# Performance work log

Hardware: AMD Instinct MI355X
Metric: run time of the kernel (lower is better)

Reference implementation:

```python
import jax, jax.numpy as jnp
import numpy as np

NUM_PRODUCT = 100000
NUM_USERS = 10000
EMBED_DIM = 512
H = EMBED_DIM // 2          # gru_hidden_size = embedding_dim // 2
MBS = 20                    # max_basket_size
NB = 64                     # baskets per user
K = 256                     # batch of users
B = NB * MBS                # flattened item positions per user
L = 2                       # GRU layers


def setup_inputs() -> dict:
    key = jax.random.key(0)
    ks = jax.random.split(key, 8)
    filter_basket_prob = jax.random.uniform(ks[0], (K, B), dtype=jnp.float32)
    # item ids in [-1, NUM_PRODUCT-1]; -1 is padding (shifted to padding_idx 0)
    input_seq_tensor = jax.random.randint(ks[1], (K, B), 0, NUM_PRODUCT + 1) - 1
    uid = jax.random.randint(ks[2], (K,), 0, NUM_USERS)
    embed_table = 0.02 * jax.random.normal(ks[3], (NUM_PRODUCT + 1, H), dtype=jnp.float32)
    embed_table = embed_table.at[0].set(0.0)  # padding_idx=0
    s = 1.0 / np.sqrt(H)
    w_ih = jax.random.uniform(ks[4], (L, 3 * H, H), jnp.float32, -s, s)
    w_hh = jax.random.uniform(ks[5], (L, 3 * H, H), jnp.float32, -s, s)
    b_ih = jax.random.uniform(ks[6], (L, 3 * H), jnp.float32, -s, s)
    b_hh = jax.random.uniform(ks[7], (L, 3 * H), jnp.float32, -s, s)
    return {"filter_basket_prob": filter_basket_prob, "input_seq_tensor": input_seq_tensor,
            "uid": uid, "embed_table": embed_table,
            "w_ih": w_ih, "w_hh": w_hh, "b_ih": b_ih, "b_hh": b_hh}


def _gru_layer(x, wih, whh, bih, bhh):
    # x: [K, T, H]; torch GRU gate math (r, z, n gate order)
    gi = jnp.einsum('kth,gh->ktg', x, wih) + bih  # [K, T, 3H]

    def step(h, gi_t):
        gh = h @ whh.T + bhh
        ir, iz, inn = jnp.split(gi_t, 3, axis=-1)
        hr, hz, hn = jnp.split(gh, 3, axis=-1)
        r = jax.nn.sigmoid(ir + hr)
        z = jax.nn.sigmoid(iz + hz)
        n = jnp.tanh(inn + r * hn)
        h_new = (1.0 - z) * n + z * h
        return h_new, h_new

    h0 = jnp.zeros((x.shape[0], whh.shape[1]), x.dtype)
    _, hs = jax.lax.scan(step, h0, jnp.swapaxes(gi, 0, 1))  # [T, K, H]
    return jnp.swapaxes(hs, 0, 1)


def reference(filter_basket_prob, input_seq_tensor, uid, embed_table, w_ih, w_hh, b_ih, b_hh):
    Kb, Bb = filter_basket_prob.shape
    Hh = embed_table.shape[1]
    nb = Bb // MBS
    # mask out padding positions (constant w.r.t. grads, as in torch .detach())
    mask = (input_seq_tensor != -1).astype(jnp.float32)
    prob = filter_basket_prob * mask                      # [K, B]
    emb = embed_table[input_seq_tensor + 1]               # [K, B, H]
    emb_f = (emb * prob[..., None]).reshape(Kb, nb, MBS, Hh)
    prob_b = prob.reshape(Kb, nb, MBS)
    filter_b = prob_b.max(axis=-1)                        # [K, NB]
    # avg basket pooling: sum(prob*emb) / (sum(prob) + eps)
    basket_emb = emb_f.sum(axis=2) / (prob_b.sum(axis=-1, keepdims=True) + 1e-10)
    valid = (filter_b > 0).astype(jnp.int32)
    # stable descending sort moves valid baskets to the front, preserving order
    order = jnp.argsort(-valid, axis=-1)                  # [K, NB]
    lengths = valid.sum(axis=-1)
    lengths = lengths + (lengths == 0).astype(lengths.dtype)  # clamp to >= 1
    x = jnp.take_along_axis(basket_emb, order[:, :, None], axis=1)  # [K, NB, H]
    # pack/pad/unsort in the original cancel out: GRU output at t depends only
    # on inputs <= t, so run the full padded scan and read step lengths-1.
    for l in range(w_ih.shape[0]):
        x = _gru_layer(x, w_ih[l], w_hh[l], b_ih[l], b_hh[l])
    return x[jnp.arange(Kb), lengths - 1]                 # [K, H]
```

## Files before the change

### kernel.cpp

```cpp
#include <hip/hip_runtime.h>
#include <cstdint>

#define KU 256
#define NBASK 64
#define MBS 20
#define BITEMS 1280
#define HD 256
#define G3 768
#define TT 64

typedef short v8s __attribute__((ext_vector_type(8)));
typedef float v4f __attribute__((ext_vector_type(4)));
typedef unsigned short v4us __attribute__((ext_vector_type(4)));
typedef unsigned int v4u __attribute__((ext_vector_type(4)));

__device__ __forceinline__ unsigned short f2b(float f){
  uint32_t u = __float_as_uint(f);
  u += 0x7FFFu + ((u >> 16) & 1u);
  return (unsigned short)(u >> 16);
}
__device__ __forceinline__ float b2f(unsigned short s){
  return __uint_as_float(((uint32_t)s) << 16);
}
__device__ __forceinline__ unsigned int packf(float x){
  unsigned short hi = f2b(x);
  unsigned short lo = f2b(x - b2f(hi));
  return ((unsigned int)hi << 16) | lo;
}
__device__ __forceinline__ float unpackf(unsigned int v){
  return b2f((unsigned short)(v >> 16)) + b2f((unsigned short)(v & 0xffffu));
}
__device__ __forceinline__ void waitflag(int* f, int v){
  while (__hip_atomic_load(f, __ATOMIC_ACQUIRE, __HIP_MEMORY_SCOPE_AGENT) < v)
    __builtin_amdgcn_s_sleep(2);
}

__global__ __launch_bounds__(1024) void k_convert(
    const float* __restrict__ wih, const float* __restrict__ whh,
    unsigned short* __restrict__ wih1hi, unsigned short* __restrict__ wih1lo,
    unsigned short* __restrict__ wih2hi, unsigned short* __restrict__ wih2lo,
    unsigned short* __restrict__ whh1hi, unsigned short* __restrict__ whh1lo,
    unsigned short* __restrict__ whh2hi, unsigned short* __restrict__ whh2lo)
{
  int idx = blockIdx.x * 1024 + threadIdx.x;
  int which = blockIdx.y;
  float v;
  if (which == 0)      v = wih[idx];
  else if (which == 1) v = wih[196608 + idx];
  else if (which == 2) v = whh[idx];
  else                 v = whh[196608 + idx];
  unsigned short hi = f2b(v);
  unsigned short lo = f2b(v - b2f(hi));
  if (which == 0)      { wih1hi[idx] = hi; wih1lo[idx] = lo; }
  else if (which == 1) { wih2hi[idx] = hi; wih2lo[idx] = lo; }
  else if (which == 2) { whh1hi[idx] = hi; whh1lo[idx] = lo; }
  else                 { whh2hi[idx] = hi; whh2lo[idx] = lo; }
}

__global__ void k_zero(int* flags){
  if (threadIdx.x < 96) flags[threadIdx.x] = 0;
}

__global__ __launch_bounds__(64) void k_order(
    const float* __restrict__ prob, const int* __restrict__ seq,
    int* __restrict__ order, int* __restrict__ lengths)
{
  int k = blockIdx.x, j = threadIdx.x;
  int base = k * BITEMS + j * MBS;
  float mx = 0.f;
  #pragma unroll
  for (int m = 0; m < MBS; m++) {
    int it = seq[base + m];
    float p = (it >= 0) ? prob[base + m] : 0.f;
    mx = fmaxf(mx, p);
  }
  bool valid = mx > 0.f;
  unsigned long long bal = __ballot(valid);
  int len = __popcll(bal);
  unsigned long long below = bal & ((1ull << j) - 1ull);
  int pos = valid ? __popcll(below) : (len + (j - __popcll(below)));
  order[k * NBASK + j] = pos;
  if (j == 0) lengths[k] = (len > 0) ? len : 1;
}

__global__ __launch_bounds__(256) void k_basket(
    const float* __restrict__ prob, const int* __restrict__ seq,
    const float* __restrict__ table, const int* __restrict__ order,
    unsigned short* __restrict__ xbhi, unsigned short* __restrict__ xblo)
{
  int j = blockIdx.x, k = blockIdx.y;
  int h = threadIdx.x;
  int base = k * BITEMS + j * MBS;
  float acc = 0.f, sp = 0.f;
  #pragma unroll
  for (int m = 0; m < MBS; m++) {
    int it = seq[base + m];
    if (it >= 0) {
      float p = prob[base + m];
      sp += p;
      acc += p * table[(size_t)(it + 1) * HD + h];
    }
  }
  float val = acc / (sp + 1e-10f);
  int dest = order[k * NBASK + j];
  unsigned short hi = f2b(val);
  size_t o = ((size_t)k * NBASK + dest) * HD + h;
  xbhi[o] = hi;
  xblo[o] = f2b(val - b2f(hi));
}

__global__ __launch_bounds__(256) void k_gemm3(
    const unsigned short* __restrict__ Xhi, const unsigned short* __restrict__ Xlo,
    const unsigned short* __restrict__ Whi, const unsigned short* __restrict__ Wlo,
    const float* __restrict__ bias, float* __restrict__ Y)
{
  int nblk = blockIdx.x;
  int mblk = blockIdx.y;
  int wv = threadIdx.x >> 6;
  int l = threadIdx.x & 63;
  int r = l & 15, g = l >> 4;
  int mbase = mblk * 64 + wv * 16;
  int nbase = nblk * 64;
  v4f acc[4];
  #pragma unroll
  for (int c = 0; c < 4; c++) {
    float bn = bias[nbase + c * 16 + r];
    acc[c] = (v4f){bn, bn, bn, bn};
  }
  const unsigned short* xh = Xhi + (size_t)(mbase + r) * HD;
  const unsigned short* xl = Xlo + (size_t)(mbase + r) * HD;
  #pragma unroll
  for (int k0 = 0; k0 < HD; k0 += 32) {
    v8s ahi = *(const v8s*)(xh + k0 + g * 8);
    v8s alo = *(const v8s*)(xl + k0 + g * 8);
    #pragma unroll
    for (int c = 0; c < 4; c++) {
      size_t wo = (size_t)(nbase + c * 16 + r) * HD + k0 + g * 8;
      v8s bhi = *(const v8s*)(Whi + wo);
      v8s blo = *(const v8s*)(Wlo + wo);
      acc[c] = __builtin_amdgcn_mfma_f32_16x16x32_bf16(ahi, bhi, acc[c], 0, 0, 0);
      acc[c] = __builtin_amdgcn_mfma_f32_16x16x32_bf16(alo, bhi, acc[c], 0, 0, 0);
      acc[c] = __builtin_amdgcn_mfma_f32_16x16x32_bf16(ahi, blo, acc[c], 0, 0, 0);
    }
  }
  #pragma unroll
  for (int c = 0; c < 4; c++) {
    int n = nbase + c * 16 + r;
    int mrow = mbase + g * 4;
    #pragma unroll
    for (int i = 0; i < 4; i++)
      Y[(size_t)(mrow + i) * G3 + n] = acc[c][i];
  }
}

__device__ __forceinline__ void wprologue(
    const unsigned short* w0, const unsigned short* w1, const unsigned short* w2,
    int half4, v8s (&cw0)[3], v8s (&cw1)[3], v8s (&cw2)[3])
{
  #pragma unroll
  for (int q = 0; q < 3; q++) {
    int p = (half4 + q) & 7;
    cw0[q] = *(const v8s*)(w0 + p * 32);
    cw1[q] = *(const v8s*)(w1 + p * 32);
    cw2[q] = *(const v8s*)(w2 + p * 32);
  }
}
template<int K0>
__device__ __forceinline__ void mfma_quad(
    const unsigned short* __restrict__ w0, const unsigned short* __restrict__ w1,
    const unsigned short* __restrict__ w2,
    const unsigned short (*h_hi)[256], const unsigned short (*h_lo)[256],
    const unsigned short* __restrict__ nlo_s, int r, int g, int jloc, int half4,
    v8s (&cw0)[3], v8s (&cw1)[3], v8s (&cw2)[3],
    v4f& a0, v4f& a1, v4f& a2)
{
  #pragma unroll
  for (int q = 0; q < 4; q++) {
    int kidx = K0 + q;
    int buf = kidx % 3;
    int p = (half4 + kidx) & 7;
    int slotA = ((p * 4 + g) ^ (r & 7)) * 8;
    v8s ahi = *(const v8s*)&h_hi[r][slotA];
    v8s alo = *(const v8s*)&h_lo[r][slotA];
    v8s nl  = *(const v8s*)&nlo_s[jloc * 256 + slotA];
    v8s u0 = cw0[buf], u1 = cw1[buf], u2 = cw2[buf];
    if (kidx + 3 < 8) {
      int p3 = (half4 + kidx + 3) & 7;
      cw0[buf] = *(const v8s*)(w0 + p3 * 32);
      cw1[buf] = *(const v8s*)(w1 + p3 * 32);
      cw2[buf] = *(const v8s*)(w2 + p3 * 32);
    }
    a0 = __builtin_amdgcn_mfma_f32_16x16x32_bf16(ahi, u0, a0, 0, 0, 0);
    a0 = __builtin_amdgcn_mfma_f32_16x16x32_bf16(alo, u0, a0, 0, 0, 0);
    a1 = __builtin_amdgcn_mfma_f32_16x16x32_bf16(ahi, u1, a1, 0, 0, 0);
    a1 = __builtin_amdgcn_mfma_f32_16x16x32_bf16(alo, u1, a1, 0, 0, 0);
    a2 = __builtin_amdgcn_mfma_f32_16x16x32_bf16(ahi, u2, a2, 0, 0, 0);
    a2 = __builtin_amdgcn_mfma_f32_16x16x32_bf16(alo, u2, a2, 0, 0, 0);
    a2 = __builtin_amdgcn_mfma_f32_16x16x32_bf16(ahi, nl, a2, 0, 0, 0);
  }
}

__global__ __launch_bounds__(512) void k_pipe(
    const unsigned short* __restrict__ whh1hi, const unsigned short* __restrict__ whh1lo,
    const unsigned short* __restrict__ wih2hi, const unsigned short* __restrict__ wih2lo,
    const unsigned short* __restrict__ whh2hi, const unsigned short* __restrict__ whh2lo,
    float* __restrict__ gi, unsigned int* __restrict__ h1pk, unsigned int* __restrict__ h2x,
    const float* __restrict__ bhh1, const float* __restrict__ bih2,
    const float* __restrict__ bhh2,
    const int* __restrict__ lengths, float* __restrict__ out, int* flags)
{
  __shared__ unsigned short h_hi[16][256], h_lo[16][256];
  __shared__ unsigned short nlo_s[40960];
  int tid = threadIdx.x;
  int l = tid & 63, r = l & 15, g = l >> 4;
  int swv = __builtin_amdgcn_readfirstlane(tid >> 6);
  int bx = blockIdx.x;
  int role = bx >> 5, sub = bx & 31, half = sub >> 4, b = sub & 15;
  int half4 = half * 4;
  int ub = b * 16;
  int jloc = swv * 16 + r, j = half * 128 + jloc;
  int* aflag = flags, *gflag = flags + 32, *bflag = flags + 64;
  int myf = sub, sibf = sub ^ 16;

  const unsigned short* whi_g = (role == 0) ? whh1hi : (role == 1) ? wih2hi : whh2hi;
  const unsigned short* wlo_g = (role == 0) ? whh1lo : (role == 1) ? wih2lo : whh2lo;
  const float* bb_ = (role == 0) ? bhh1 : (role == 1) ? bih2 : bhh2;

  for (int idx = tid; idx < 4096; idx += 512) {
    ((unsigned short*)h_hi)[idx] = 0;
    ((unsigned short*)h_lo)[idx] = 0;
  }
  const unsigned short* wlo_n = wlo_g + 2 * 65536 + half * 128 * 256;
  for (int idx = tid; idx < 32768; idx += 512) {
    int row = idx >> 8, col = idx & 255;
    int slot = (col >> 3) ^ (row & 7);
    nlo_s[row * 256 + slot * 8 + (col & 7)] = wlo_n[idx];
  }
  const unsigned short* w0 = whi_g + (size_t)j * 256 + g * 8;
  const unsigned short* w1 = w0 + 65536;
  const unsigned short* w2 = w0 + 131072;
  float b_r = bb_[j], b_z = bb_[256 + j], b_n = bb_[512 + j];
  int sibbase = (1 - half) * 128;
  int xu = tid >> 5;
  __syncthreads();

  if (role == 0) {
    float hold[4] = {0.f, 0.f, 0.f, 0.f};
    const float* gp[4];
    unsigned int* hq[4];
    #pragma unroll
    for (int i = 0; i < 4; i++) {
      gp[i] = gi + (size_t)(ub + g * 4 + i) * TT * G3 + j;
      hq[i] = h1pk + (size_t)(ub + g * 4 + i) * TT * HD + j;
    }
    for (int t = 0; t < TT; t++) {
      float gir[4], giz[4], gin[4];
      #pragma unroll
      for (int i = 0; i < 4; i++) {
        gir[i] = gp[i][0]; giz[i] = gp[i][256]; gin[i] = gp[i][512];
        gp[i] += G3;
      }
      v8s cw0[3], cw1[3], cw2[3];
      wprologue(w0, w1, w2, half4, cw0, cw1, cw2);
      v4f a0 = {0.f,0.f,0.f,0.f}, a1 = {0.f,0.f,0.f,0.f}, a2 = {0.f,0.f,0.f,0.f};
      mfma_quad<0>(w0, w1, w2, h_hi, h_lo, nlo_s, r, g, jloc, half4, cw0, cw1, cw2, a0, a1, a2);
      if (t > 0 && tid == 0) waitflag(&aflag[sibf], t);
      __syncthreads();
      if (t > 0) {
        int sj = sibbase + (tid & 31) * 4;
        v4u pk = *(const v4u*)&h1pk[((size_t)(ub + xu) * TT + (t - 1)) * HD + sj];
        int pos = (((sj >> 3) ^ (xu & 7)) << 3) + (sj & 7);
        v4us hv, lv;
        #pragma unroll
        for (int i = 0; i < 4; i++) { hv[i] = (unsigned short)(pk[i] >> 16); lv[i] = (unsigned short)(pk[i] & 0xffffu); }
        *(v4us*)&h_hi[xu][pos] = hv;
        *(v4us*)&h_lo[xu][pos] = lv;
      }
      __syncthreads();
      mfma_quad<4>(w0, w1, w2, h_hi, h_lo, nlo_s, r, g, jloc, half4, cw0, cw1, cw2, a0, a1, a2);
      #pragma unroll
      for (int i = 0; i < 4; i++) {
        float hr = a0[i] + b_r, hz = a1[i] + b_z, hn = a2[i] + b_n;
        float rr = 1.f / (1.f + __expf(-(gir[i] + hr)));
        float zz = 1.f / (1.f + __expf(-(giz[i] + hz)));
        float e  = __expf(2.f * (gin[i] + rr * hn));
        float nn = 1.f - 2.f / (e + 1.f);
        float hnew = (1.f - zz) * nn + zz * hold[i];
        hold[i] = hnew;
        unsigned short h_  = f2b(hnew);
        unsigned short lo_ = f2b(hnew - b2f(h_));
        int u = g * 4 + i;
        int pos = (((j >> 3) ^ (u & 7)) << 3) + (j & 7);
        h_hi[u][pos] = h_;
        h_lo[u][pos] = lo_;
        hq[i][0] = ((unsigned int)h_ << 16) | lo_;
        hq[i] += HD;
      }
      __syncthreads();
      if (tid == 0) {
        __threadfence();
        __hip_atomic_store(&aflag[myf], t + 1, __ATOMIC_RELEASE, __HIP_MEMORY_SCOPE_AGENT);
      }
    }
  } else if (role == 1) {
    unsigned int* gi_u = (unsigned int*)gi;
    for (int t = 0; t < TT; t++) {
      if (tid == 0) { waitflag(&aflag[b], t + 1); waitflag(&aflag[16 + b], t + 1); }
      __syncthreads();
      {
        int c0 = (tid & 31) * 8;
        const unsigned int* src = &h1pk[((size_t)(ub + xu) * TT + t) * HD + c0];
        #pragma unroll
        for (int hf = 0; hf < 2; hf++) {
          v4u pk = *(const v4u*)(src + hf * 4);
          int sj = c0 + hf * 4;
          int pos = (((sj >> 3) ^ (xu & 7)) << 3) + (sj & 7);
          v4us hv, lv;
          #pragma unroll
          for (int i = 0; i < 4; i++) { hv[i] = (unsigned short)(pk[i] >> 16); lv[i] = (unsigned short)(pk[i] & 0xffffu); }
          *(v4us*)&h_hi[xu][pos] = hv;
          *(v4us*)&h_lo[xu][pos] = lv;
        }
      }
      __syncthreads();
      v8s cw0[3], cw1[3], cw2[3];
      wprologue(w0, w1, w2, half4, cw0, cw1, cw2);
      v4f a0 = {b_r, b_r, b_r, b_r}, a1 = {b_z, b_z, b_z, b_z}, a2 = {b_n, b_n, b_n, b_n};
      mfma_quad<0>(w0, w1, w2, h_hi, h_lo, nlo_s, r, g, jloc, half4, cw0, cw1, cw2, a0, a1, a2);
      mfma_quad<4>(w0, w1, w2, h_hi, h_lo, nlo_s, r, g, jloc, half4, cw0, cw1, cw2, a0, a1, a2);
      #pragma unroll
      for (int i = 0; i < 4; i++) {
        size_t base = ((size_t)(ub + g * 4 + i) * TT + t) * G3;
        gi_u[base + j]       = packf(a0[i]);
        gi_u[base + 256 + j] = packf(a1[i]);
        gi_u[base + 512 + j] = packf(a2[i]);
      }
      __syncthreads();
      if (tid == 0) {
        __threadfence();
        __hip_atomic_store(&gflag[myf], t + 1, __ATOMIC_RELEASE, __HIP_MEMORY_SCOPE_AGENT);
      }
    }
  } else {
    float hold[4] = {0.f, 0.f, 0.f, 0.f};
    const unsigned int* gq[4];
    int lenr[4];
    #pragma unroll
    for (int i = 0; i < 4; i++) {
      gq[i] = (const unsigned int*)gi + (size_t)(ub + g * 4 + i) * TT * G3 + j;
      lenr[i] = lengths[ub + g * 4 + i];
    }
    for (int t = 0; t < TT; t++) {
      v8s cw0[3], cw1[3], cw2[3];
      wprologue(w0, w1, w2, half4, cw0, cw1, cw2);
      v4f a0 = {0.f,0.f,0.f,0.f}, a1 = {0.f,0.f,0.f,0.f}, a2 = {0.f,0.f,0.f,0.f};
      mfma_quad<0>(w0, w1, w2, h_hi, h_lo, nlo_s, r, g, jloc, half4, cw0, cw1, cw2, a0, a1, a2);
      if (tid == 0) {
        waitflag(&gflag[myf], t + 1);
        if (t > 0) waitflag(&bflag[sibf], t);
      }
      __syncthreads();
      if (t > 0) {
        int sj = sibbase + (tid & 31) * 4;
        v4u pk = *(const v4u*)&h2x[(size_t)(ub + xu) * HD + sj];
        int pos = (((sj >> 3) ^ (xu & 7)) << 3) + (sj & 7);
        v4us hv, lv;
        #pragma unroll
        for (int i = 0; i < 4; i++) { hv[i] = (unsigned short)(pk[i] >> 16); lv[i] = (unsigned short)(pk[i] & 0xffffu); }
        *(v4us*)&h_hi[xu][pos] = hv;
        *(v4us*)&h_lo[xu][pos] = lv;
      }
      unsigned int vr[4], vz[4], vn[4];
      #pragma unroll
      for (int i = 0; i < 4; i++) {
        vr[i] = gq[i][0]; vz[i] = gq[i][256]; vn[i] = gq[i][512];
        gq[i] += G3;
      }
      __syncthreads();
      mfma_quad<4>(w0, w1, w2, h_hi, h_lo, nlo_s, r, g, jloc, half4, cw0, cw1, cw2, a0, a1, a2);
      #pragma unroll
      for (int i = 0; i < 4; i++) {
        float hr = a0[i] + b_r, hz = a1[i] + b_z, hn = a2[i] + b_n;
        float rr = 1.f / (1.f + __expf(-(unpackf(vr[i]) + hr)));
        float zz = 1.f / (1.f + __expf(-(unpackf(vz[i]) + hz)));
        float e  = __expf(2.f * (unpackf(vn[i]) + rr * hn));
        float nn = 1.f - 2.f / (e + 1.f);
        float hnew = (1.f - zz) * nn + zz * hold[i];
        hold[i] = hnew;
        unsigned short h_  = f2b(hnew);
        unsigned short lo_ = f2b(hnew - b2f(h_));
        int u = g * 4 + i;
        int pos = (((j >> 3) ^ (u & 7)) << 3) + (j & 7);
        h_hi[u][pos] = h_;
        h_lo[u][pos] = lo_;
        h2x[(size_t)(ub + u) * HD + j] = ((unsigned int)h_ << 16) | lo_;
        if (t == lenr[i] - 1)
          out[(size_t)(ub + u) * HD + j] = hnew;
      }
      __syncthreads();
      if (tid == 0) {
        __threadfence();
        __hip_atomic_store(&bflag[myf], t + 1, __ATOMIC_RELEASE, __HIP_MEMORY_SCOPE_AGENT);
      }
    }
  }
}

extern "C" void kernel_launch(void* const* d_in, const int* in_sizes, int n_in,
                              void* d_out, int out_size, void* d_ws, size_t ws_size,
                              hipStream_t stream) {
  const float* prob  = (const float*)d_in[0];
  const int*   seq   = (const int*)d_in[1];
  const float* table = (const float*)d_in[3];
  const float* wih   = (const float*)d_in[4];
  const float* whh   = (const float*)d_in[5];
  const float* bih   = (const float*)d_in[6];
  const float* bhh   = (const float*)d_in[7];
  float* out = (float*)d_out;

  char* ws = (char*)d_ws;
  float* gi            = (float*)ws;
  unsigned short* xbhi = (unsigned short*)(ws + 50331648);
  unsigned short* xblo = (unsigned short*)(ws + 58720256);
  unsigned int* h1pk   = (unsigned int*)xbhi;
  char* wsw = ws + 67108864;
  const size_t WSZ = 393216;
  unsigned short* wih1hi = (unsigned short*)(wsw + 0 * WSZ);
  unsigned short* wih1lo = (unsigned short*)(wsw + 1 * WSZ);
  unsigned short* wih2hi = (unsigned short*)(wsw + 2 * WSZ);
  unsigned short* wih2lo = (unsigned short*)(wsw + 3 * WSZ);
  unsigned short* whh1hi = (unsigned short*)(wsw + 4 * WSZ);
  unsigned short* whh1lo = (unsigned short*)(wsw + 5 * WSZ);
  unsigned short* whh2hi = (unsigned short*)(wsw + 6 * WSZ);
  unsigned short* whh2lo = (unsigned short*)(wsw + 7 * WSZ);
  int* order   = (int*)(wsw + 8 * WSZ);
  int* lengths = order + KU * NBASK;
  int* flags   = lengths + KU;
  unsigned int* h2x = (unsigned int*)wih1hi;

  k_zero<<<1, 128, 0, stream>>>(flags);
  k_convert<<<dim3(192, 4), 1024, 0, stream>>>(wih, whh,
      wih1hi, wih1lo, wih2hi, wih2lo, whh1hi, whh1lo, whh2hi, whh2lo);
  k_order<<<dim3(KU), 64, 0, stream>>>(prob, seq, order, lengths);
  k_basket<<<dim3(NBASK, KU), 256, 0, stream>>>(prob, seq, table, order, xbhi, xblo);
  k_gemm3<<<dim3(12, 256), 256, 0, stream>>>(xbhi, xblo, wih1hi, wih1lo, bih, gi);
  k_pipe<<<dim3(96), 512, 0, stream>>>(
      whh1hi, whh1lo, wih2hi, wih2lo, whh2hi, whh2lo,
      gi, h1pk, h2x, bhh, bih + G3, bhh + G3, lengths, out, flags);
}
```

Before: 712.3 us.

## Relax inter-block flag sync and prefetch layer-1 input gates into LDS

Replaces acquire loads and explicit threadfences around the cross-block flags with relaxed polling plus release stores, and reads producer data through relaxed agent-scope atomic loads instead. Layer-1 blocks now prefetch the next timestep's input-gate rows into a double-buffered shared-memory tile with coalesced vector loads, replacing per-lane strided global reads. The aim is to shorten the serial per-step latency of the pipelined GRU recurrence. Relying on relaxed ordering carries a risk of memory-ordering races, and the larger LDS footprint may affect occupancy.

```diff
diff --git a/kernel.cpp b/kernel.cpp
--- a/kernel.cpp
+++ b/kernel.cpp
@@ -31,8 +31,12 @@
   return b2f((unsigned short)(v >> 16)) + b2f((unsigned short)(v & 0xffffu));
 }
 __device__ __forceinline__ void waitflag(int* f, int v){
-  while (__hip_atomic_load(f, __ATOMIC_ACQUIRE, __HIP_MEMORY_SCOPE_AGENT) < v)
+  while (__hip_atomic_load(f, __ATOMIC_RELAXED, __HIP_MEMORY_SCOPE_AGENT) < v)
     __builtin_amdgcn_s_sleep(2);
+  asm volatile("" ::: "memory");
+}
+__device__ __forceinline__ unsigned int aload(const unsigned int* p){
+  return __hip_atomic_load(p, __ATOMIC_RELAXED, __HIP_MEMORY_SCOPE_AGENT);
 }
 
 __global__ __launch_bounds__(1024) void k_convert(
@@ -200,6 +204,28 @@
   }
 }
 
+__device__ __forceinline__ void load_gi(
+    const float* __restrict__ gi, int ub, int t, int half, int tid,
+    float (*gs)[388])
+{
+  v4f tmp[3];
+  #pragma unroll
+  for (int k = 0; k < 3; k++) {
+    int idx = k * 512 + tid;
+    int row = idx >> 5, c4 = idx & 31;
+    int u = row / 3, gate = row - u * 3;
+    tmp[k] = *(const v4f*)(gi + ((size_t)(ub + u) * TT + t) * G3
+                              + gate * 256 + half * 128 + c4 * 4);
+  }
+  #pragma unroll
+  for (int k = 0; k < 3; k++) {
+    int idx = k * 512 + tid;
+    int row = idx >> 5, c4 = idx & 31;
+    int u = row / 3, gate = row - u * 3;
+    *(v4f*)&gs[u][gate * 128 + c4 * 4] = tmp[k];
+  }
+}
+
 __global__ __launch_bounds__(512) void k_pipe(
     const unsigned short* __restrict__ whh1hi, const unsigned short* __restrict__ whh1lo,
     const unsigned short* __restrict__ wih2hi, const unsigned short* __restrict__ wih2lo,
@@ -210,7 +236,8 @@
     const int* __restrict__ lengths, float* __restrict__ out, int* flags)
 {
   __shared__ unsigned short h_hi[16][256], h_lo[16][256];
-  __shared__ unsigned short nlo_s[40960];
+  __shared__ unsigned short nlo_s[32768];
+  __shared__ float gi_s[2][16][388];
   int tid = threadIdx.x;
   int l = tid & 63, r = l & 15, g = l >> 4;
   int swv = __builtin_amdgcn_readfirstlane(tid >> 6);
@@ -246,20 +273,13 @@
 
   if (role == 0) {
     float hold[4] = {0.f, 0.f, 0.f, 0.f};
-    const float* gp[4];
     unsigned int* hq[4];
     #pragma unroll
-    for (int i = 0; i < 4; i++) {
-      gp[i] = gi + (size_t)(ub + g * 4 + i) * TT * G3 + j;
+    for (int i = 0; i < 4; i++)
       hq[i] = h1pk + (size_t)(ub + g * 4 + i) * TT * HD + j;
-    }
+    load_gi(gi, ub, 0, half, tid, gi_s[0]);
+    __syncthreads();
     for (int t = 0; t < TT; t++) {
-      float gir[4], giz[4], gin[4];
-      #pragma unroll
-      for (int i = 0; i < 4; i++) {
-        gir[i] = gp[i][0]; giz[i] = gp[i][256]; gin[i] = gp[i][512];
-        gp[i] += G3;
-      }
       v8s cw0[3], cw1[3], cw2[3];
       wprologue(w0, w1, w2, half4, cw0, cw1, cw2);
       v4f a0 = {0.f,0.f,0.f,0.f}, a1 = {0.f,0.f,0.f,0.f}, a2 = {0.f,0.f,0.f,0.f};
@@ -278,18 +298,22 @@
       }
       __syncthreads();
       mfma_quad<4>(w0, w1, w2, h_hi, h_lo, nlo_s, r, g, jloc, half4, cw0, cw1, cw2, a0, a1, a2);
+      if (t + 1 < TT) load_gi(gi, ub, t + 1, half, tid, gi_s[(t + 1) & 1]);
       #pragma unroll
       for (int i = 0; i < 4; i++) {
+        int u = g * 4 + i;
+        float ir  = gi_s[t & 1][u][jloc];
+        float iz  = gi_s[t & 1][u][128 + jloc];
+        float inn = gi_s[t & 1][u][256 + jloc];
         float hr = a0[i] + b_r, hz = a1[i] + b_z, hn = a2[i] + b_n;
-        float rr = 1.f / (1.f + __expf(-(gir[i] + hr)));
-        float zz = 1.f / (1.f + __expf(-(giz[i] + hz)));
-        float e  = __expf(2.f * (gin[i] + rr * hn));
+        float rr = 1.f / (1.f + __expf(-(ir + hr)));
+        float zz = 1.f / (1.f + __expf(-(iz + hz)));
+        float e  = __expf(2.f * (inn + rr * hn));
         float nn = 1.f - 2.f / (e + 1.f);
         float hnew = (1.f - zz) * nn + zz * hold[i];
         hold[i] = hnew;
         unsigned short h_  = f2b(hnew);
         unsigned short lo_ = f2b(hnew - b2f(h_));
-        int u = g * 4 + i;
         int pos = (((j >> 3) ^ (u & 7)) << 3) + (j & 7);
         h_hi[u][pos] = h_;
         h_lo[u][pos] = lo_;
@@ -297,10 +321,8 @@
         hq[i] += HD;
       }
       __syncthreads();
-      if (tid == 0) {
-        __threadfence();
+      if (tid == 0)
         __hip_atomic_store(&aflag[myf], t + 1, __ATOMIC_RELEASE, __HIP_MEMORY_SCOPE_AGENT);
-      }
     }
   } else if (role == 1) {
     unsigned int* gi_u = (unsigned int*)gi;
@@ -336,10 +358,8 @@
         gi_u[base + 512 + j] = packf(a2[i]);
       }
       __syncthreads();
-      if (tid == 0) {
-        __threadfence();
+      if (tid == 0)
         __hip_atomic_store(&gflag[myf], t + 1, __ATOMIC_RELEASE, __HIP_MEMORY_SCOPE_AGENT);
-      }
     }
   } else {
     float hold[4] = {0.f, 0.f, 0.f, 0.f};
@@ -362,18 +382,21 @@
       __syncthreads();
       if (t > 0) {
         int sj = sibbase + (tid & 31) * 4;
-        v4u pk = *(const v4u*)&h2x[(size_t)(ub + xu) * HD + sj];
+        const unsigned int* hx = &h2x[(size_t)(ub + xu) * HD + sj];
+        unsigned int p0 = aload(hx), p1 = aload(hx + 1), p2 = aload(hx + 2), p3 = aload(hx + 3);
         int pos = (((sj >> 3) ^ (xu & 7)) << 3) + (sj & 7);
         v4us hv, lv;
-        #pragma unroll
-        for (int i = 0; i < 4; i++) { hv[i] = (unsigned short)(pk[i] >> 16); lv[i] = (unsigned short)(pk[i] & 0xffffu); }
+        hv[0]=(unsigned short)(p0>>16); lv[0]=(unsigned short)(p0&0xffffu);
+        hv[1]=(unsigned short)(p1>>16); lv[1]=(unsigned short)(p1&0xffffu);
+        hv[2]=(unsigned short)(p2>>16); lv[2]=(unsigned short)(p2&0xffffu);
+        hv[3]=(unsigned short)(p3>>16); lv[3]=(unsigned short)(p3&0xffffu);
         *(v4us*)&h_hi[xu][pos] = hv;
         *(v4us*)&h_lo[xu][pos] = lv;
       }
       unsigned int vr[4], vz[4], vn[4];
       #pragma unroll
       for (int i = 0; i < 4; i++) {
-        vr[i] = gq[i][0]; vz[i] = gq[i][256]; vn[i] = gq[i][512];
+        vr[i] = aload(gq[i]); vz[i] = aload(gq[i] + 256); vn[i] = aload(gq[i] + 512);
         gq[i] += G3;
       }
       __syncthreads();
@@ -398,10 +421,8 @@
           out[(size_t)(ub + u) * HD + j] = hnew;
       }
       __syncthreads();
-      if (tid == 0) {
-        __threadfence();
+      if (tid == 0)
         __hip_atomic_store(&bflag[myf], t + 1, __ATOMIC_RELEASE, __HIP_MEMORY_SCOPE_AGENT);
-      }
     }
   }
 }
```

New measurement: 744.8 us. 1.05x slower.

## Split GRU pipeline K-reduction across two wave groups with LDS partial-sum merge

Applied to the files above, without the earlier changes.

The persistent pipelined GRU kernel goes from 512 to 1024 threads per block. Each recurrent matvec's K dimension is split between a front and a back group of 8 waves, and the back group's partial accumulators are reduced through a new LDS buffer before the front group does the gate math. Loading the sibling hidden state is handed to the back waves, which overlaps it with the front waves' work. The layer-2 hidden exchange buffer is double-buffered by timestep parity. This aims to shorten the serial per-step latency, at the cost of an extra __syncthreads, LDS traffic per step, and higher register pressure under launch_bounds(1024).

```diff
diff --git a/kernel.cpp b/kernel.cpp
--- a/kernel.cpp
+++ b/kernel.cpp
@@ -153,54 +153,26 @@
   }
 }
 
-__device__ __forceinline__ void wprologue(
-    const unsigned short* w0, const unsigned short* w1, const unsigned short* w2,
-    int half4, v8s (&cw0)[3], v8s (&cw1)[3], v8s (&cw2)[3])
-{
-  #pragma unroll
-  for (int q = 0; q < 3; q++) {
-    int p = (half4 + q) & 7;
-    cw0[q] = *(const v8s*)(w0 + p * 32);
-    cw1[q] = *(const v8s*)(w1 + p * 32);
-    cw2[q] = *(const v8s*)(w2 + p * 32);
-  }
-}
-template<int K0>
-__device__ __forceinline__ void mfma_quad(
-    const unsigned short* __restrict__ w0, const unsigned short* __restrict__ w1,
-    const unsigned short* __restrict__ w2,
+__device__ __forceinline__ void mfma_one(
+    int p, v8s u0, v8s u1, v8s u2,
     const unsigned short (*h_hi)[256], const unsigned short (*h_lo)[256],
-    const unsigned short* __restrict__ nlo_s, int r, int g, int jloc, int half4,
-    v8s (&cw0)[3], v8s (&cw1)[3], v8s (&cw2)[3],
+    const unsigned short* __restrict__ nlo_s, int r, int g, int jloc,
     v4f& a0, v4f& a1, v4f& a2)
 {
-  #pragma unroll
-  for (int q = 0; q < 4; q++) {
-    int kidx = K0 + q;
-    int buf = kidx % 3;
-    int p = (half4 + kidx) & 7;
-    int slotA = ((p * 4 + g) ^ (r & 7)) * 8;
-    v8s ahi = *(const v8s*)&h_hi[r][slotA];
-    v8s alo = *(const v8s*)&h_lo[r][slotA];
-    v8s nl  = *(const v8s*)&nlo_s[jloc * 256 + slotA];
-    v8s u0 = cw0[buf], u1 = cw1[buf], u2 = cw2[buf];
-    if (kidx + 3 < 8) {
-      int p3 = (half4 + kidx + 3) & 7;
-      cw0[buf] = *(const v8s*)(w0 + p3 * 32);
-      cw1[buf] = *(const v8s*)(w1 + p3 * 32);
-      cw2[buf] = *(const v8s*)(w2 + p3 * 32);
-    }
-    a0 = __builtin_amdgcn_mfma_f32_16x16x32_bf16(ahi, u0, a0, 0, 0, 0);
-    a0 = __builtin_amdgcn_mfma_f32_16x16x32_bf16(alo, u0, a0, 0, 0, 0);
-    a1 = __builtin_amdgcn_mfma_f32_16x16x32_bf16(ahi, u1, a1, 0, 0, 0);
-    a1 = __builtin_amdgcn_mfma_f32_16x16x32_bf16(alo, u1, a1, 0, 0, 0);
-    a2 = __builtin_amdgcn_mfma_f32_16x16x32_bf16(ahi, u2, a2, 0, 0, 0);
-    a2 = __builtin_amdgcn_mfma_f32_16x16x32_bf16(alo, u2, a2, 0, 0, 0);
-    a2 = __builtin_amdgcn_mfma_f32_16x16x32_bf16(ahi, nl, a2, 0, 0, 0);
-  }
-}
-
-__global__ __launch_bounds__(512) void k_pipe(
+  int slotA = ((p * 4 + g) ^ (r & 7)) * 8;
+  v8s ahi = *(const v8s*)&h_hi[r][slotA];
+  v8s alo = *(const v8s*)&h_lo[r][slotA];
+  v8s nl  = *(const v8s*)&nlo_s[jloc * 256 + slotA];
+  a0 = __builtin_amdgcn_mfma_f32_16x16x32_bf16(ahi, u0, a0, 0, 0, 0);
+  a0 = __builtin_amdgcn_mfma_f32_16x16x32_bf16(alo, u0, a0, 0, 0, 0);
+  a1 = __builtin_amdgcn_mfma_f32_16x16x32_bf16(ahi, u1, a1, 0, 0, 0);
+  a1 = __builtin_amdgcn_mfma_f32_16x16x32_bf16(alo, u1, a1, 0, 0, 0);
+  a2 = __builtin_amdgcn_mfma_f32_16x16x32_bf16(ahi, u2, a2, 0, 0, 0);
+  a2 = __builtin_amdgcn_mfma_f32_16x16x32_bf16(alo, u2, a2, 0, 0, 0);
+  a2 = __builtin_amdgcn_mfma_f32_16x16x32_bf16(ahi, nl, a2, 0, 0, 0);
+}
+
+__global__ __launch_bounds__(1024) void k_pipe(
     const unsigned short* __restrict__ whh1hi, const unsigned short* __restrict__ whh1lo,
     const unsigned short* __restrict__ wih2hi, const unsigned short* __restrict__ wih2lo,
     const unsigned short* __restrict__ whh2hi, const unsigned short* __restrict__ whh2lo,
@@ -210,28 +182,32 @@
     const int* __restrict__ lengths, float* __restrict__ out, int* flags)
 {
   __shared__ unsigned short h_hi[16][256], h_lo[16][256];
-  __shared__ unsigned short nlo_s[40960];
+  __shared__ unsigned short nlo_s[32768];
+  __shared__ float pacc[8 * 3 * 292];
   int tid = threadIdx.x;
   int l = tid & 63, r = l & 15, g = l >> 4;
   int swv = __builtin_amdgcn_readfirstlane(tid >> 6);
+  bool front = swv < 8;
+  int cswv = swv & 7;
   int bx = blockIdx.x;
   int role = bx >> 5, sub = bx & 31, half = sub >> 4, b = sub & 15;
   int half4 = half * 4;
   int ub = b * 16;
-  int jloc = swv * 16 + r, j = half * 128 + jloc;
+  int jloc = cswv * 16 + r, j = half * 128 + jloc;
   int* aflag = flags, *gflag = flags + 32, *bflag = flags + 64;
   int myf = sub, sibf = sub ^ 16;
+  int loff = l * 4 + (l >> 3) * 4;
 
   const unsigned short* whi_g = (role == 0) ? whh1hi : (role == 1) ? wih2hi : whh2hi;
   const unsigned short* wlo_g = (role == 0) ? whh1lo : (role == 1) ? wih2lo : whh2lo;
   const float* bb_ = (role == 0) ? bhh1 : (role == 1) ? bih2 : bhh2;
 
-  for (int idx = tid; idx < 4096; idx += 512) {
+  for (int idx = tid; idx < 4096; idx += 1024) {
     ((unsigned short*)h_hi)[idx] = 0;
     ((unsigned short*)h_lo)[idx] = 0;
   }
   const unsigned short* wlo_n = wlo_g + 2 * 65536 + half * 128 * 256;
-  for (int idx = tid; idx < 32768; idx += 512) {
+  for (int idx = tid; idx < 32768; idx += 1024) {
     int row = idx >> 8, col = idx & 255;
     int slot = (col >> 3) ^ (row & 7);
     nlo_s[row * 256 + slot * 8 + (col & 7)] = wlo_n[idx];
@@ -241,7 +217,13 @@
   const unsigned short* w2 = w0 + 131072;
   float b_r = bb_[j], b_z = bb_[256 + j], b_n = bb_[512 + j];
   int sibbase = (1 - half) * 128;
-  int xu = tid >> 5;
+  int bt = tid - 512;
+  int xu = bt >> 5;
+  int kA0, kA1, kA2, kA3;
+  if (role == 1) { kA0 = front ? 0 : 4; kA1 = kA0 + 1; kA2 = kA0 + 2; kA3 = kA0 + 3; }
+  else           { kA0 = front ? 0 : 2; kA1 = kA0 + 1; kA2 = front ? 4 : 6; kA3 = kA2 + 1; }
+  int p0 = (half4 + kA0) & 7, p1 = (half4 + kA1) & 7;
+  int p2 = (half4 + kA2) & 7, p3 = (half4 + kA3) & 7;
   __syncthreads();
 
   if (role == 0) {
@@ -254,20 +236,25 @@
       hq[i] = h1pk + (size_t)(ub + g * 4 + i) * TT * HD + j;
     }
     for (int t = 0; t < TT; t++) {
+      v8s c00 = *(const v8s*)(w0 + p0*32), c10 = *(const v8s*)(w1 + p0*32), c20 = *(const v8s*)(w2 + p0*32);
+      v8s c01 = *(const v8s*)(w0 + p1*32), c11 = *(const v8s*)(w1 + p1*32), c21 = *(const v8s*)(w2 + p1*32);
+      v8s c02 = *(const v8s*)(w0 + p2*32), c12 = *(const v8s*)(w1 + p2*32), c22 = *(const v8s*)(w2 + p2*32);
+      v8s c03 = *(const v8s*)(w0 + p3*32), c13 = *(const v8s*)(w1 + p3*32), c23 = *(const v8s*)(w2 + p3*32);
       float gir[4], giz[4], gin[4];
-      #pragma unroll
-      for (int i = 0; i < 4; i++) {
-        gir[i] = gp[i][0]; giz[i] = gp[i][256]; gin[i] = gp[i][512];
-        gp[i] += G3;
-      }
-      v8s cw0[3], cw1[3], cw2[3];
-      wprologue(w0, w1, w2, half4, cw0, cw1, cw2);
+      if (front) {
+        #pragma unroll
+        for (int i = 0; i < 4; i++) {
+          gir[i] = gp[i][0]; giz[i] = gp[i][256]; gin[i] = gp[i][512];
+          gp[i] += G3;
+        }
+      }
       v4f a0 = {0.f,0.f,0.f,0.f}, a1 = {0.f,0.f,0.f,0.f}, a2 = {0.f,0.f,0.f,0.f};
-      mfma_quad<0>(w0, w1, w2, h_hi, h_lo, nlo_s, r, g, jloc, half4, cw0, cw1, cw2, a0, a1, a2);
-      if (t > 0 && tid == 0) waitflag(&aflag[sibf], t);
-      __syncthreads();
-      if (t > 0) {
-        int sj = sibbase + (tid & 31) * 4;
+      mfma_one(p0, c00, c10, c20, h_hi, h_lo, nlo_s, r, g, jloc, a0, a1, a2);
+      mfma_one(p1, c01, c11, c21, h_hi, h_lo, nlo_s, r, g, jloc, a0, a1, a2);
+      if (t > 0 && tid == 512) waitflag(&aflag[sibf], t);
+      __syncthreads();
+      if (!front && t > 0) {
+        int sj = sibbase + (bt & 31) * 4;
         v4u pk = *(const v4u*)&h1pk[((size_t)(ub + xu) * TT + (t - 1)) * HD + sj];
         int pos = (((sj >> 3) ^ (xu & 7)) << 3) + (sj & 7);
         v4us hv, lv;
@@ -277,24 +264,36 @@
         *(v4us*)&h_lo[xu][pos] = lv;
       }
       __syncthreads();
-      mfma_quad<4>(w0, w1, w2, h_hi, h_lo, nlo_s, r, g, jloc, half4, cw0, cw1, cw2, a0, a1, a2);
-      #pragma unroll
-      for (int i = 0; i < 4; i++) {
-        float hr = a0[i] + b_r, hz = a1[i] + b_z, hn = a2[i] + b_n;
-        float rr = 1.f / (1.f + __expf(-(gir[i] + hr)));
-        float zz = 1.f / (1.f + __expf(-(giz[i] + hz)));
-        float e  = __expf(2.f * (gin[i] + rr * hn));
-        float nn = 1.f - 2.f / (e + 1.f);
-        float hnew = (1.f - zz) * nn + zz * hold[i];
-        hold[i] = hnew;
-        unsigned short h_  = f2b(hnew);
-        unsigned short lo_ = f2b(hnew - b2f(h_));
-        int u = g * 4 + i;
-        int pos = (((j >> 3) ^ (u & 7)) << 3) + (j & 7);
-        h_hi[u][pos] = h_;
-        h_lo[u][pos] = lo_;
-        hq[i][0] = ((unsigned int)h_ << 16) | lo_;
-        hq[i] += HD;
+      mfma_one(p2, c02, c12, c22, h_hi, h_lo, nlo_s, r, g, jloc, a0, a1, a2);
+      mfma_one(p3, c03, c13, c23, h_hi, h_lo, nlo_s, r, g, jloc, a0, a1, a2);
+      if (!front) {
+        *(v4f*)&pacc[(cswv * 3 + 0) * 292 + loff] = a0;
+        *(v4f*)&pacc[(cswv * 3 + 1) * 292 + loff] = a1;
+        *(v4f*)&pacc[(cswv * 3 + 2) * 292 + loff] = a2;
+      }
+      __syncthreads();
+      if (front) {
+        a0 += *(const v4f*)&pacc[(cswv * 3 + 0) * 292 + loff];
+        a1 += *(const v4f*)&pacc[(cswv * 3 + 1) * 292 + loff];
+        a2 += *(const v4f*)&pacc[(cswv * 3 + 2) * 292 + loff];
+        #pragma unroll
+        for (int i = 0; i < 4; i++) {
+          float hr = a0[i] + b_r, hz = a1[i] + b_z, hn = a2[i] + b_n;
+          float rr = 1.f / (1.f + __expf(-(gir[i] + hr)));
+          float zz = 1.f / (1.f + __expf(-(giz[i] + hz)));
+          float e  = __expf(2.f * (gin[i] + rr * hn));
+          float nn = 1.f - 2.f / (e + 1.f);
+          float hnew = (1.f - zz) * nn + zz * hold[i];
+          hold[i] = hnew;
+          unsigned short h_  = f2b(hnew);
+          unsigned short lo_ = f2b(hnew - b2f(h_));
+          int u = g * 4 + i;
+          int pos = (((j >> 3) ^ (u & 7)) << 3) + (j & 7);
+          h_hi[u][pos] = h_;
+          h_lo[u][pos] = lo_;
+          hq[i][0] = ((unsigned int)h_ << 16) | lo_;
+          hq[i] += HD;
+        }
       }
       __syncthreads();
       if (tid == 0) {
@@ -304,36 +303,48 @@
     }
   } else if (role == 1) {
     unsigned int* gi_u = (unsigned int*)gi;
+    int gxu = tid >> 6, gc0 = (tid & 63) * 4;
     for (int t = 0; t < TT; t++) {
-      if (tid == 0) { waitflag(&aflag[b], t + 1); waitflag(&aflag[16 + b], t + 1); }
+      v8s c00 = *(const v8s*)(w0 + p0*32), c10 = *(const v8s*)(w1 + p0*32), c20 = *(const v8s*)(w2 + p0*32);
+      v8s c01 = *(const v8s*)(w0 + p1*32), c11 = *(const v8s*)(w1 + p1*32), c21 = *(const v8s*)(w2 + p1*32);
+      v8s c02 = *(const v8s*)(w0 + p2*32), c12 = *(const v8s*)(w1 + p2*32), c22 = *(const v8s*)(w2 + p2*32);
+      v8s c03 = *(const v8s*)(w0 + p3*32), c13 = *(const v8s*)(w1 + p3*32), c23 = *(const v8s*)(w2 + p3*32);
+      if (tid == 512) { waitflag(&aflag[b], t + 1); waitflag(&aflag[16 + b], t + 1); }
       __syncthreads();
       {
-        int c0 = (tid & 31) * 8;
-        const unsigned int* src = &h1pk[((size_t)(ub + xu) * TT + t) * HD + c0];
-        #pragma unroll
-        for (int hf = 0; hf < 2; hf++) {
-          v4u pk = *(const v4u*)(src + hf * 4);
-          int sj = c0 + hf * 4;
-          int pos = (((sj >> 3) ^ (xu & 7)) << 3) + (sj & 7);
-          v4us hv, lv;
-          #pragma unroll
-          for (int i = 0; i < 4; i++) { hv[i] = (unsigned short)(pk[i] >> 16); lv[i] = (unsigned short)(pk[i] & 0xffffu); }
-          *(v4us*)&h_hi[xu][pos] = hv;
-          *(v4us*)&h_lo[xu][pos] = lv;
+        v4u pk = *(const v4u*)&h1pk[((size_t)(ub + gxu) * TT + t) * HD + gc0];
+        int pos = (((gc0 >> 3) ^ (gxu & 7)) << 3) + (gc0 & 7);
+        v4us hv, lv;
+        #pragma unroll
+        for (int i = 0; i < 4; i++) { hv[i] = (unsigned short)(pk[i] >> 16); lv[i] = (unsigned short)(pk[i] & 0xffffu); }
+        *(v4us*)&h_hi[gxu][pos] = hv;
+        *(v4us*)&h_lo[gxu][pos] = lv;
+      }
+      __syncthreads();
+      v4f a0, a1, a2;
+      if (front) { a0 = (v4f){b_r,b_r,b_r,b_r}; a1 = (v4f){b_z,b_z,b_z,b_z}; a2 = (v4f){b_n,b_n,b_n,b_n}; }
+      else       { a0 = (v4f){0.f,0.f,0.f,0.f}; a1 = a0; a2 = a0; }
+      mfma_one(p0, c00, c10, c20, h_hi, h_lo, nlo_s, r, g, jloc, a0, a1, a2);
+      mfma_one(p1, c01, c11, c21, h_hi, h_lo, nlo_s, r, g, jloc, a0, a1, a2);
+      mfma_one(p2, c02, c12, c22, h_hi, h_lo, nlo_s, r, g, jloc, a0, a1, a2);
+      mfma_one(p3, c03, c13, c23, h_hi, h_lo, nlo_s, r, g, jloc, a0, a1, a2);
+      if (!front) {
+        *(v4f*)&pacc[(cswv * 3 + 0) * 292 + loff] = a0;
+        *(v4f*)&pacc[(cswv * 3 + 1) * 292 + loff] = a1;
+        *(v4f*)&pacc[(cswv * 3 + 2) * 292 + loff] = a2;
+      }
+      __syncthreads();
+      if (front) {
+        a0 += *(const v4f*)&pacc[(cswv * 3 + 0) * 292 + loff];
+        a1 += *(const v4f*)&pacc[(cswv * 3 + 1) * 292 + loff];
+        a2 += *(const v4f*)&pacc[(cswv * 3 + 2) * 292 + loff];
+        #pragma unroll
+        for (int i = 0; i < 4; i++) {
+          size_t base = ((size_t)(ub + g * 4 + i) * TT + t) * G3;
+          gi_u[base + j]       = packf(a0[i]);
+          gi_u[base + 256 + j] = packf(a1[i]);
+          gi_u[base + 512 + j] = packf(a2[i]);
         }
-      }
-      __syncthreads();
-      v8s cw0[3], cw1[3], cw2[3];
-      wprologue(w0, w1, w2, half4, cw0, cw1, cw2);
-      v4f a0 = {b_r, b_r, b_r, b_r}, a1 = {b_z, b_z, b_z, b_z}, a2 = {b_n, b_n, b_n, b_n};
-      mfma_quad<0>(w0, w1, w2, h_hi, h_lo, nlo_s, r, g, jloc, half4, cw0, cw1, cw2, a0, a1, a2);
-      mfma_quad<4>(w0, w1, w2, h_hi, h_lo, nlo_s, r, g, jloc, half4, cw0, cw1, cw2, a0, a1, a2);
-      #pragma unroll
-      for (int i = 0; i < 4; i++) {
-        size_t base = ((size_t)(ub + g * 4 + i) * TT + t) * G3;
-        gi_u[base + j]       = packf(a0[i]);
-        gi_u[base + 256 + j] = packf(a1[i]);
-        gi_u[base + 512 + j] = packf(a2[i]);
       }
       __syncthreads();
       if (tid == 0) {
@@ -344,25 +355,29 @@
   } else {
     float hold[4] = {0.f, 0.f, 0.f, 0.f};
     const unsigned int* gq[4];
-    int lenr[4];
+    int lenr[4] = {0, 0, 0, 0};
     #pragma unroll
     for (int i = 0; i < 4; i++) {
       gq[i] = (const unsigned int*)gi + (size_t)(ub + g * 4 + i) * TT * G3 + j;
-      lenr[i] = lengths[ub + g * 4 + i];
+      if (front) lenr[i] = lengths[ub + g * 4 + i];
     }
     for (int t = 0; t < TT; t++) {
-      v8s cw0[3], cw1[3], cw2[3];
-      wprologue(w0, w1, w2, half4, cw0, cw1, cw2);
+      v8s c00 = *(const v8s*)(w0 + p0*32), c10 = *(const v8s*)(w1 + p0*32), c20 = *(const v8s*)(w2 + p0*32);
+      v8s c01 = *(const v8s*)(w0 + p1*32), c11 = *(const v8s*)(w1 + p1*32), c21 = *(const v8s*)(w2 + p1*32);
+      v8s c02 = *(const v8s*)(w0 + p2*32), c12 = *(const v8s*)(w1 + p2*32), c22 = *(const v8s*)(w2 + p2*32);
+      v8s c03 = *(const v8s*)(w0 + p3*32), c13 = *(const v8s*)(w1 + p3*32), c23 = *(const v8s*)(w2 + p3*32);
       v4f a0 = {0.f,0.f,0.f,0.f}, a1 = {0.f,0.f,0.f,0.f}, a2 = {0.f,0.f,0.f,0.f};
-      mfma_quad<0>(w0, w1, w2, h_hi, h_lo, nlo_s, r, g, jloc, half4, cw0, cw1, cw2, a0, a1, a2);
-      if (tid == 0) {
+      mfma_one(p0, c00, c10, c20, h_hi, h_lo, nlo_s, r, g, jloc, a0, a1, a2);
+      mfma_one(p1, c01, c11, c21, h_hi, h_lo, nlo_s, r, g, jloc, a0, a1, a2);
+      if (tid == 512) {
         waitflag(&gflag[myf], t + 1);
         if (t > 0) waitflag(&bflag[sibf], t);
       }
       __syncthreads();
-      if (t > 0) {
-        int sj = sibbase + (tid & 31) * 4;
-        v4u pk = *(const v4u*)&h2x[(size_t)(ub + xu) * HD + sj];
+      unsigned int vr[4], vz[4], vn[4];
+      if (!front && t > 0) {
+        int sj = sibbase + (bt & 31) * 4;
+        v4u pk = *(const v4u*)&h2x[((t - 1) & 1) * 65536 + (ub + xu) * HD + sj];
         int pos = (((sj >> 3) ^ (xu & 7)) << 3) + (sj & 7);
         v4us hv, lv;
         #pragma unroll
@@ -370,32 +385,45 @@
         *(v4us*)&h_hi[xu][pos] = hv;
         *(v4us*)&h_lo[xu][pos] = lv;
       }
-      unsigned int vr[4], vz[4], vn[4];
-      #pragma unroll
-      for (int i = 0; i < 4; i++) {
-        vr[i] = gq[i][0]; vz[i] = gq[i][256]; vn[i] = gq[i][512];
-        gq[i] += G3;
-      }
-      __syncthreads();
-      mfma_quad<4>(w0, w1, w2, h_hi, h_lo, nlo_s, r, g, jloc, half4, cw0, cw1, cw2, a0, a1, a2);
-      #pragma unroll
-      for (int i = 0; i < 4; i++) {
-        float hr = a0[i] + b_r, hz = a1[i] + b_z, hn = a2[i] + b_n;
-        float rr = 1.f / (1.f + __expf(-(unpackf(vr[i]) + hr)));
-        float zz = 1.f / (1.f + __expf(-(unpackf(vz[i]) + hz)));
-        float e  = __expf(2.f * (unpackf(vn[i]) + rr * hn));
-        float nn = 1.f - 2.f / (e + 1.f);
-        float hnew = (1.f - zz) * nn + zz * hold[i];
-        hold[i] = hnew;
-        unsigned short h_  = f2b(hnew);
-        unsigned short lo_ = f2b(hnew - b2f(h_));
-        int u = g * 4 + i;
-        int pos = (((j >> 3) ^ (u & 7)) << 3) + (j & 7);
-        h_hi[u][pos] = h_;
-        h_lo[u][pos] = lo_;
-        h2x[(size_t)(ub + u) * HD + j] = ((unsigned int)h_ << 16) | lo_;
-        if (t == lenr[i] - 1)
-          out[(size_t)(ub + u) * HD + j] = hnew;
+      if (front) {
+        #pragma unroll
+        for (int i = 0; i < 4; i++) {
+          vr[i] = gq[i][0]; vz[i] = gq[i][256]; vn[i] = gq[i][512];
+          gq[i] += G3;
+        }
+      }
+      __syncthreads();
+      mfma_one(p2, c02, c12, c22, h_hi, h_lo, nlo_s, r, g, jloc, a0, a1, a2);
+      mfma_one(p3, c03, c13, c23, h_hi, h_lo, nlo_s, r, g, jloc, a0, a1, a2);
+      if (!front) {
+        *(v4f*)&pacc[(cswv * 3 + 0) * 292 + loff] = a0;
+        *(v4f*)&pacc[(cswv * 3 + 1) * 292 + loff] = a1;
+        *(v4f*)&pacc[(cswv * 3 + 2) * 292 + loff] = a2;
+      }
+      __syncthreads();
+      if (front) {
+        a0 += *(const v4f*)&pacc[(cswv * 3 + 0) * 292 + loff];
+        a1 += *(const v4f*)&pacc[(cswv * 3 + 1) * 292 + loff];
+        a2 += *(const v4f*)&pacc[(cswv * 3 + 2) * 292 + loff];
+        #pragma unroll
+        for (int i = 0; i < 4; i++) {
+          float hr = a0[i] + b_r, hz = a1[i] + b_z, hn = a2[i] + b_n;
+          float rr = 1.f / (1.f + __expf(-(unpackf(vr[i]) + hr)));
+          float zz = 1.f / (1.f + __expf(-(unpackf(vz[i]) + hz)));
+          float e  = __expf(2.f * (unpackf(vn[i]) + rr * hn));
+          float nn = 1.f - 2.f / (e + 1.f);
+          float hnew = (1.f - zz) * nn + zz * hold[i];
+          hold[i] = hnew;
+          unsigned short h_  = f2b(hnew);
+          unsigned short lo_ = f2b(hnew - b2f(h_));
+          int u = g * 4 + i;
+          int pos = (((j >> 3) ^ (u & 7)) << 3) + (j & 7);
+          h_hi[u][pos] = h_;
+          h_lo[u][pos] = lo_;
+          h2x[(t & 1) * 65536 + (ub + u) * HD + j] = ((unsigned int)h_ << 16) | lo_;
+          if (t == lenr[i] - 1)
+            out[(size_t)(ub + u) * HD + j] = hnew;
+        }
       }
       __syncthreads();
       if (tid == 0) {
@@ -444,7 +472,7 @@
   k_order<<<dim3(KU), 64, 0, stream>>>(prob, seq, order, lengths);
   k_basket<<<dim3(NBASK, KU), 256, 0, stream>>>(prob, seq, table, order, xbhi, xblo);
   k_gemm3<<<dim3(12, 256), 256, 0, stream>>>(xbhi, xblo, wih1hi, wih1lo, bih, gi);
-  k_pipe<<<dim3(96), 512, 0, stream>>>(
+  k_pipe<<<dim3(96), 1024, 0, stream>>>(
       whh1hi, whh1lo, wih2hi, wih2lo, whh2hi, whh2lo,
       gi, h1pk, h2x, bhh, bih + G3, bhh + G3, lengths, out, flags);
 }
```

After: 846.8 us. 18.9% more time.
